# Performance work log

Hardware: AMD Instinct MI355X
Metric: run time of the kernel (lower is better)

## Reference

```python
import jax, jax.numpy as jnp
import numpy as np

N, E, H = 50000, 800000, 128
NUM_NC = 40
NUM_LAYERS = 3


def setup_inputs() -> dict:
    key = jax.random.key(0)
    ks = jax.random.split(key, 16)
    s = 1.0 / np.sqrt(H)
    inp = {
        "x": jax.random.normal(ks[0], (N, H), jnp.float32),
        "edge_index": jax.random.randint(ks[1], (2, E), 0, N, jnp.int64),
        "na_alphas": 0.001 * jax.random.normal(ks[2], (3, 4), jnp.float32),
        "sc_alphas": 0.001 * jax.random.normal(ks[3], (2, 2), jnp.float32),
        "la_alphas": 0.001 * jax.random.normal(ks[4], (1, 3), jnp.float32),
        "lin1_W": s * jax.random.normal(ks[5], (H, H), jnp.float32),
        "lin1_b": jnp.zeros((H,), jnp.float32),
        "gcn_W": s * jax.random.normal(ks[6], (3, H, H), jnp.float32),
        "gcn_b": jnp.zeros((3, H), jnp.float32),
        "sage_Ws": s * jax.random.normal(ks[7], (3, H, H), jnp.float32),
        "sage_Wn": s * jax.random.normal(ks[8], (3, H, H), jnp.float32),
        "gin_W": s * jax.random.normal(ks[9], (3, H, H), jnp.float32),
        "gin_b": jnp.zeros((3, H), jnp.float32),
        "gin_eps": jnp.zeros((3,), jnp.float32),
        "gat_W": s * jax.random.normal(ks[10], (3, H, H), jnp.float32),
        "gat_as": s * jax.random.normal(ks[11], (3, H), jnp.float32),
        "gat_ad": s * jax.random.normal(ks[12], (3, H), jnp.float32),
        "nc_W": s * jax.random.normal(ks[13], (NUM_NC, H), jnp.float32),
        "nc_b": jnp.zeros((NUM_NC,), jnp.float32),
    }
    return inp


def _gcn(x, src, dst, deg_inv_sqrt, W, b):
    h = x @ W.T + b                           # [N, H]
    norm = deg_inv_sqrt[src] * deg_inv_sqrt[dst]
    msg = h[src] * norm[:, None]              # [E, H] gather
    return jax.ops.segment_sum(msg, dst, num_segments=N)


def _sage(x, src, dst, deg, Ws, Wn):
    agg = jax.ops.segment_sum(x[src], dst, num_segments=N) / jnp.maximum(deg, 1.0)[:, None]
    return x @ Ws.T + agg @ Wn.T


def _gin(x, src, dst, W, b, eps):
    agg = jax.ops.segment_sum(x[src], dst, num_segments=N)
    return ((1.0 + eps) * x + agg) @ W.T + b


def _gat(x, src, dst, W, a_s, a_d):
    h = x @ W.T                               # [N, H]
    logits = jax.nn.leaky_relu((h @ a_s)[src] + (h @ a_d)[dst], 0.2)  # [E]
    m = jax.ops.segment_max(logits, dst, num_segments=N)
    e = jnp.exp(logits - m[dst])
    z = jax.ops.segment_sum(e, dst, num_segments=N)
    alpha = e / (z[dst] + 1e-16)
    return jax.ops.segment_sum(alpha[:, None] * h[src], dst, num_segments=N)


def _na_mixed(x, w, src, dst, deg, dis, l, gcn_W, gcn_b, sage_Ws, sage_Wn,
              gin_W, gin_b, gin_eps, gat_W, gat_as, gat_ad):
    # sum_i w_i * elu(op_i(x, edge_index))
    o0 = _gcn(x, src, dst, dis, gcn_W[l], gcn_b[l])
    o1 = _sage(x, src, dst, deg, sage_Ws[l], sage_Wn[l])
    o2 = _gin(x, src, dst, gin_W[l], gin_b[l], gin_eps[l])
    o3 = _gat(x, src, dst, gat_W[l], gat_as[l], gat_ad[l])
    return (w[0] * jax.nn.elu(o0) + w[1] * jax.nn.elu(o1)
            + w[2] * jax.nn.elu(o2) + w[3] * jax.nn.elu(o3))


def reference(x, edge_index, na_alphas, sc_alphas, la_alphas, lin1_W, lin1_b,
              gcn_W, gcn_b, sage_Ws, sage_Wn, gin_W, gin_b, gin_eps,
              gat_W, gat_as, gat_ad, nc_W, nc_b):
    src, dst = edge_index[0], edge_index[1]
    deg = jax.ops.segment_sum(jnp.ones((E,), x.dtype), dst, num_segments=N)
    dis = jnp.where(deg > 0, 1.0 / jnp.sqrt(jnp.maximum(deg, 1.0)), 0.0)

    na_w = jax.nn.softmax(na_alphas, axis=-1)   # [3, 4]
    sc_w = jax.nn.softmax(sc_alphas, axis=-1)   # [2, 2] (none, skip)
    la_w = jax.nn.softmax(la_alphas, axis=-1)   # [1, 3]

    h = x @ lin1_W.T + lin1_b                   # dropout: eval mode -> identity
    xs = []
    cur = h
    for l in range(NUM_LAYERS):
        cur = _na_mixed(cur, na_w[l], src, dst, deg, dis, l, gcn_W, gcn_b,
                        sage_Ws, sage_Wn, gin_W, gin_b, gin_eps,
                        gat_W, gat_as, gat_ad)
        xs.append(cur)
    x1, x2, x3 = xs

    # fix_last=True: x4 = (x3, sc0(x1), sc1(x2)); SC ops = {none->0, skip->id}
    t = jnp.stack([x3, sc_w[0, 1] * x1, sc_w[1, 1] * x2], axis=0)  # [3, N, H]

    # layer aggregator: sum_i w_i * relu(op_i(tuple)); ops = {max, mean, sum}
    x5 = (la_w[0, 0] * jax.nn.relu(jnp.max(t, axis=0))
          + la_w[0, 1] * jax.nn.relu(jnp.mean(t, axis=0))
          + la_w[0, 2] * jax.nn.relu(jnp.sum(t, axis=0)))

    return x5 @ nc_W.T + nc_b                   # [N, NUM_NC]
```

## Files before the change

kernel.cpp:

```cpp
#include <hip/hip_runtime.h>
#include <hip/hip_bf16.h>

typedef unsigned short u16;
typedef unsigned int u32;
typedef __attribute__((ext_vector_type(8))) short short8;
typedef __attribute__((ext_vector_type(4))) float f32x4;
typedef __attribute__((ext_vector_type(2))) float f32x2;

#define HD 128
#define ETILE 8192

__device__ inline float b2f(u16 u){ u32 v = ((u32)u) << 16; return __uint_as_float(v); }
__device__ inline u16 f2b(float f){
  u32 u = __float_as_uint(f);
  u32 r = (u + 0x7fffu + ((u >> 16) & 1u)) >> 16;
  return (u16)r;
}
__device__ inline u32 pack2(float a, float b){
  __hip_bfloat162 h = __float22bfloat162_rn(make_float2(a, b));
  union { __hip_bfloat162 h; u32 u; } c; c.h = h; return c.u;
}
__device__ inline float lo2f(u32 w){ return b2f((u16)(w & 0xffff)); }
__device__ inline float hi2f(u32 w){ return b2f((u16)(w >> 16)); }
__device__ inline float eluf(float x){ return x > 0.f ? x : __expf(x) - 1.f; }
__device__ inline float reluf(float x){ return x > 0.f ? x : 0.f; }
__device__ inline float sane(float x){
  if (!(x == x)) return 0.f;
  return fminf(fmaxf(x, -1e30f), 1e30f);
}
__device__ inline u32 fenc(float f){ u32 u = __float_as_uint(f); return (u & 0x80000000u) ? ~u : (u | 0x80000000u); }
__device__ inline float fdec(u32 u){ return __uint_as_float((u & 0x80000000u) ? (u & 0x7fffffffu) : ~u); }
__device__ __forceinline__ void async16(const u16* g, u16* l){
  __builtin_amdgcn_global_load_lds((const __attribute__((address_space(1))) void*)g,
                                   (__attribute__((address_space(3))) void*)l, 16, 0, 0);
}

__global__ void k_small(const float* __restrict__ na_a, const float* __restrict__ sc_a,
                        const float* __restrict__ la_a, const float* __restrict__ gatW,
                        const float* __restrict__ gat_as, const float* __restrict__ gat_ad,
                        const float* __restrict__ gin_eps, float* __restrict__ sm,
                        u32* __restrict__ maxs)
{
  int t = threadIdx.x;
  if (t < 3) maxs[t] = 0u;
  if (t == 0){
    for (int l = 0; l < 3; l++){
      float a[4]; float mx = -1e30f;
      for (int i = 0; i < 4; i++){ a[i] = na_a[l*4+i]; mx = fmaxf(mx, a[i]); }
      float ssum = 0.f;
      for (int i = 0; i < 4; i++){ a[i] = __expf(a[i]-mx); ssum += a[i]; }
      for (int i = 0; i < 4; i++) sm[l*4+i] = a[i]/ssum;
    }
    for (int r = 0; r < 2; r++){
      float a0 = sc_a[r*2], a1 = sc_a[r*2+1];
      float mx = fmaxf(a0,a1);
      float e0 = __expf(a0-mx), e1 = __expf(a1-mx);
      sm[12+r] = e1/(e0+e1);
    }
    {
      float a0=la_a[0], a1=la_a[1], a2=la_a[2];
      float mx = fmaxf(fmaxf(a0,a1),a2);
      float e0=__expf(a0-mx), e1=__expf(a1-mx), e2=__expf(a2-mx);
      float ssum = e0+e1+e2;
      sm[14]=e0/ssum; sm[15]=e1/ssum; sm[16]=e2/ssum;
    }
    for (int l=0;l<3;l++) sm[17+l] = 1.f + gin_eps[l];
  }
  if (t < 128){
    for (int l=0;l<3;l++){
      float a1=0.f, a2=0.f;
      for (int k=0;k<128;k++){
        float wv = gatW[l*16384 + k*128 + t];
        a1 = fmaf(wv, gat_as[l*128+k], a1);
        a2 = fmaf(wv, gat_ad[l*128+k], a2);
      }
      sm[32  + l*128 + t] = a1;
      sm[416 + l*128 + t] = a2;
    }
  }
}

__device__ __forceinline__ uint4 cvt8(const float* __restrict__ p){
  float4 v0 = *(const float4*)p;
  float4 v1 = *(const float4*)(p + 4);
  uint4 o;
  o.x = pack2(v0.x, v0.y);
  o.y = pack2(v0.z, v0.w);
  o.z = pack2(v1.x, v1.y);
  o.w = pack2(v1.z, v1.w);
  return o;
}
__global__ void k_wcvt(const float* __restrict__ lin1W, const float* __restrict__ gcnW,
                       const float* __restrict__ Ws, const float* __restrict__ Wn,
                       const float* __restrict__ ginW, const float* __restrict__ gatW,
                       u16* __restrict__ wsb)
{
  int i = blockIdx.x*256 + threadIdx.x;
  if (i >= 32768) return;
  int m = i >> 11;
  int j = i & 2047;
  int r = j >> 4, c = j & 15;
  const float* src;
  if (m == 0)       src = lin1W;
  else if (m < 4)   src = gcnW + (m-1)*16384;
  else if (m < 7)   src = Ws   + (m-4)*16384;
  else if (m < 10)  src = Wn   + (m-7)*16384;
  else if (m < 13)  src = ginW + (m-10)*16384;
  else              src = gatW + (m-13)*16384;
  int dj = r*16 + (c ^ (r & 15));
  *(uint4*)(wsb + ((size_t)m*2048 + dj)*8) = cvt8(src + r*HD + c*8);
}


__global__ void k_ehist(const int* __restrict__ ei, int E, int* __restrict__ eh){
  __shared__ int h[256];
  int t = threadIdx.x, b = blockIdx.x;
  h[t] = 0; __syncthreads();
  int base = b*ETILE;
  #pragma unroll
  for (int r = 0; r < ETILE/256; r++){
    int e = base + r*256 + t;
    if (e < E) atomicAdd(&h[ei[E + e] >> 8], 1);
  }
  __syncthreads();
  eh[b*256 + t] = h[t];
}
__global__ void k_escan(int* __restrict__ eh, int nblk, int* __restrict__ btot){
  __shared__ int s[256];
  int b = blockIdx.x, t = threadIdx.x;
  int carry = 0;
  int rounds = (nblk + 255)/256;
  for (int r = 0; r < rounds; r++){
    int i = r*256 + t;
    int v = (i < nblk) ? eh[i*256 + b] : 0;
    s[t] = v; __syncthreads();
    for (int off = 1; off < 256; off <<= 1){
      int a = (t >= off) ? s[t - off] : 0;
      __syncthreads();
      s[t] += a;
      __syncthreads();
    }
    if (i < nblk) eh[i*256 + b] = s[t] - v + carry;
    carry += s[255];
    __syncthreads();
  }
  if (t == 0) btot[b] = carry;
}
__global__ void k_bscan(const int* __restrict__ btot, int B, int E, int* __restrict__ bbase){
  __shared__ int s[256];
  int t = threadIdx.x;
  int v = (t < B) ? btot[t] : 0;
  s[t] = v; __syncthreads();
  for (int off = 1; off < 256; off <<= 1){
    int a = (t >= off) ? s[t - off] : 0;
    __syncthreads();
    s[t] += a;
    __syncthreads();
  }
  if (t < B) bbase[t] = s[t] - v;
  if (t == 0) bbase[B] = E;
}
__global__ void k_escat(const int* __restrict__ ei, int E, int B,
                        const int* __restrict__ eh, const int* __restrict__ bbase,
                        int2* __restrict__ ebuf){
  __shared__ int cur[256];
  int t = threadIdx.x, b = blockIdx.x;
  cur[t] = (t < B) ? bbase[t] + eh[b*256 + t] : 0;
  __syncthreads();
  int base = b*ETILE;
  #pragma unroll
  for (int r = 0; r < ETILE/256; r++){
    int e = base + r*256 + t;
    if (e < E){
      int sv = ei[e], dv = ei[E + e];
      int p = atomicAdd(&cur[dv >> 8], 1);
      ebuf[p] = make_int2(sv, dv);
    }
  }
}
__global__ void k_bcount(const int2* __restrict__ ebuf, const int* __restrict__ bbase,
                         int Nn, int* __restrict__ cnt){
  __shared__ int c[256];
  int t = threadIdx.x, b = blockIdx.x;
  c[t] = 0; __syncthreads();
  int beg = bbase[b], end2 = bbase[b+1];
  for (int i = beg + t; i < end2; i += 256)
    atomicAdd(&c[ebuf[i].y & 255], 1);
  __syncthreads();
  int node = b*256 + t;
  if (node < Nn) cnt[node] = c[t];
}
__global__ void k_bfill(const int2* __restrict__ ebuf, const int* __restrict__ bbase,
                        const int* __restrict__ rowptr, int Nn, int* __restrict__ csr){
  __shared__ int cu[256];
  int t = threadIdx.x, b = blockIdx.x;
  int node = b*256 + t;
  cu[t] = (node < Nn) ? rowptr[node] : 0;
  __syncthreads();
  int beg = bbase[b], end2 = bbase[b+1];
  for (int i = beg + t; i < end2; i += 256){
    int2 ed = ebuf[i];
    int p = atomicAdd(&cu[ed.y & 255], 1);
    csr[p] = ed.x;
  }
}

__global__ void k_scan1(const int* __restrict__ cnt, int Nn, int* __restrict__ bsum){
  __shared__ int red[256];
  int b = blockIdx.x, t = threadIdx.x;
  int base = b*1024 + t*4;
  int s = 0;
  #pragma unroll
  for (int k = 0; k < 4; k++){ int i = base + k; if (i < Nn) s += cnt[i]; }
  red[t] = s; __syncthreads();
  for (int off = 128; off; off >>= 1){
    if (t < off) red[t] += red[t + off];
    __syncthreads();
  }
  if (t == 0) bsum[b] = red[0];
}

__global__ void k_scan2(const int* __restrict__ bsum, int nb,
                        int* __restrict__ boffs, int* __restrict__ rowptr, int Nn){
  __shared__ int sc[1024];
  int t = threadIdx.x;
  int own = (t < nb) ? bsum[t] : 0;
  sc[t] = own;
  __syncthreads();
  for (int off = 1; off < 1024; off <<= 1){
    int add = (t >= off) ? sc[t - off] : 0;
    __syncthreads();
    sc[t] += add;
    __syncthreads();
  }
  if (t < nb) boffs[t] = sc[t] - own;
  if (t == 1023) rowptr[Nn] = sc[1023];
}

__global__ void k_scan3(const int* __restrict__ cnt, const int* __restrict__ boffs, int Nn,
                        int* __restrict__ rowptr, float4* __restrict__ nd){
  __shared__ int red[256];
  int b = blockIdx.x, t = threadIdx.x;
  int base = b*1024 + t*4;
  int c[4]; int s = 0;
  #pragma unroll
  for (int k = 0; k < 4; k++){ int i = base + k; c[k] = (i < Nn) ? cnt[i] : 0; s += c[k]; }
  red[t] = s; __syncthreads();
  for (int off = 1; off < 256; off <<= 1){
    int add = (t >= off) ? red[t - off] : 0;
    __syncthreads();
    red[t] += add;
    __syncthreads();
  }
  int run = red[t] - s + boffs[b];
  #pragma unroll
  for (int k = 0; k < 4; k++){
    int i = base + k;
    if (i < Nn){
      rowptr[i] = run;
      float f = (float)c[k];
      nd[i].z = c[k] > 0 ? 1.f/sqrtf(f) : 0.f;
      nd[i].w = 1.f/fmaxf(f, 1.f);
      run += c[k];
    }
  }
}

__global__ void k_histblk(const int* __restrict__ cnt, int Nn, int* __restrict__ bh){
  __shared__ int h[256];
  int t = threadIdx.x, b = blockIdx.x;
  h[t] = 0; __syncthreads();
  int base = b*1024;
  #pragma unroll
  for (int k = 0; k < 4; k++){
    int i = base + t + k*256;
    if (i < Nn){ int d = cnt[i]; if (d > 255) d = 255; atomicAdd(&h[d], 1); }
  }
  __syncthreads();
  bh[b*256 + t] = h[t];
}
__global__ void k_hsscan(int* __restrict__ bh, int nb){
  __shared__ int tot[256];
  __shared__ int sc[256];
  int t = threadIdx.x;
  int s = 0;
  for (int b = 0; b < nb; b++){
    int v = bh[b*256 + t];
    bh[b*256 + t] = s;
    s += v;
  }
  tot[t] = s;
  int rt = 255 - t;
  __syncthreads();
  sc[rt] = tot[t];
  __syncthreads();
  for (int off = 1; off < 256; off <<= 1){
    int a = (rt >= off) ? sc[rt - off] : 0;
    __syncthreads();
    sc[rt] += a;
    __syncthreads();
  }
  int binbase = sc[rt] - tot[t];
  for (int b = 0; b < nb; b++) bh[b*256 + t] += binbase;
}
__global__ void k_permscat(const int* __restrict__ cnt, int Nn,
                           const int* __restrict__ bh, int* __restrict__ perm){
  __shared__ int cur[256];
  int t = threadIdx.x, b = blockIdx.x;
  cur[t] = bh[b*256 + t];
  __syncthreads();
  int base = b*1024;
  #pragma unroll
  for (int k = 0; k < 4; k++){
    int i = base + t + k*256;
    if (i < Nn){
      int d = cnt[i]; if (d > 255) d = 255;
      int p = atomicAdd(&cur[d], 1);
      perm[p] = i;
    }
  }
}

__global__ __launch_bounds__(256)
void k_agg(const u16* __restrict__ X, const int* __restrict__ rowptr, const int* __restrict__ csr,
           const int* __restrict__ perm,
           const float4* __restrict__ nd, const float* __restrict__ sm,
           const u32* __restrict__ maxs, int layer, int Nn,
           u16* __restrict__ Qb, u16* __restrict__ Pm, u16* __restrict__ Gb, u16* __restrict__ Rb,
           float* __restrict__ b0)
{
  int tid = threadIdx.x;
  int lane = tid & 63;
  int g = lane >> 4, t = lane & 15;
  int idx = blockIdx.x*16 + (tid >> 6)*4 + g;
  if (idx >= Nn) return;
  int wv = perm[idx];
  int beg = rowptr[wv], end = rowptr[wv+1];
  float4 ndw = nd[wv];
  float dval = ndw.y;
  float bnd = fdec(maxs[layer]) + dval;
  float mloc = fmaxf(bnd, 0.2f*bnd);
  f32x2 p2[4], q2[4], r2[4];
  #pragma unroll
  for (int k = 0; k < 4; k++){ p2[k] = (f32x2){0.f,0.f}; q2[k] = (f32x2){0.f,0.f}; r2[k] = (f32x2){0.f,0.f}; }
  float z = 0.f, qd = 0.f;
  int e = beg;
  int nsv0=0, nsv1=0, nsv2=0, nsv3=0;
  if (e + 3 < end){ nsv0 = csr[e]; nsv1 = csr[e+1]; nsv2 = csr[e+2]; nsv3 = csr[e+3]; }
  while (e + 3 < end){
    int sv0 = nsv0, sv1 = nsv1, sv2 = nsv2, sv3 = nsv3;
    int en = e + 4;
    if (en + 3 < end){ nsv0 = csr[en]; nsv1 = csr[en+1]; nsv2 = csr[en+2]; nsv3 = csr[en+3]; }
    float4 n0 = nd[sv0], n1 = nd[sv1], n2 = nd[sv2], n3 = nd[sv3];
    uint4 xv0 = *(const uint4*)(X + (size_t)sv0*HD + (t ^ (sv0 & 15))*8);
    uint4 xv1 = *(const uint4*)(X + (size_t)sv1*HD + (t ^ (sv1 & 15))*8);
    uint4 xv2 = *(const uint4*)(X + (size_t)sv2*HD + (t ^ (sv2 & 15))*8);
    uint4 xv3 = *(const uint4*)(X + (size_t)sv3*HD + (t ^ (sv3 & 15))*8);
    float s0 = n0.x + dval, s1 = n1.x + dval, s2 = n2.x + dval, s3 = n3.x + dval;
    float lg0 = fmaxf(s0, 0.2f*s0), lg1 = fmaxf(s1, 0.2f*s1);
    float lg2 = fmaxf(s2, 0.2f*s2), lg3 = fmaxf(s3, 0.2f*s3);
    float ew0 = __expf(lg0 - mloc), ew1 = __expf(lg1 - mloc);
    float ew2 = __expf(lg2 - mloc), ew3 = __expf(lg3 - mloc);
    u32 a0[4] = {xv0.x, xv0.y, xv0.z, xv0.w};
    u32 a1[4] = {xv1.x, xv1.y, xv1.z, xv1.w};
    u32 a2[4] = {xv2.x, xv2.y, xv2.z, xv2.w};
    u32 a3[4] = {xv3.x, xv3.y, xv3.z, xv3.w};
    f32x2 d0 = {n0.z, n0.z}, d1 = {n1.z, n1.z}, d2 = {n2.z, n2.z}, d3 = {n3.z, n3.z};
    f32x2 e0 = {ew0, ew0}, e1v = {ew1, ew1}, e2v = {ew2, ew2}, e3v = {ew3, ew3};
    #pragma unroll
    for (int k = 0; k < 4; k++){
      f32x2 xf0 = {lo2f(a0[k]), hi2f(a0[k])};
      f32x2 xf1 = {lo2f(a1[k]), hi2f(a1[k])};
      f32x2 xf2 = {lo2f(a2[k]), hi2f(a2[k])};
      f32x2 xf3 = {lo2f(a3[k]), hi2f(a3[k])};
      p2[k] += (xf0 + xf1) + (xf2 + xf3);
      q2[k] = __builtin_elementwise_fma(xf0, d0, q2[k]);
      q2[k] = __builtin_elementwise_fma(xf1, d1, q2[k]);
      q2[k] = __builtin_elementwise_fma(xf2, d2, q2[k]);
      q2[k] = __builtin_elementwise_fma(xf3, d3, q2[k]);
      r2[k] = __builtin_elementwise_fma(xf0, e0, r2[k]);
      r2[k] = __builtin_elementwise_fma(xf1, e1v, r2[k]);
      r2[k] = __builtin_elementwise_fma(xf2, e2v, r2[k]);
      r2[k] = __builtin_elementwise_fma(xf3, e3v, r2[k]);
    }
    z += (ew0 + ew1) + (ew2 + ew3);
    qd += (n0.z + n1.z) + (n2.z + n3.z);
    e = en;
  }
  if (e + 1 < end){
    int sv0 = csr[e], sv1 = csr[e+1];
    float4 n0 = nd[sv0], n1 = nd[sv1];
    uint4 xv0 = *(const uint4*)(X + (size_t)sv0*HD + (t ^ (sv0 & 15))*8);
    uint4 xv1 = *(const uint4*)(X + (size_t)sv1*HD + (t ^ (sv1 & 15))*8);
    float s0 = n0.x + dval, s1 = n1.x + dval;
    float lg0 = fmaxf(s0, 0.2f*s0);
    float lg1 = fmaxf(s1, 0.2f*s1);
    float ew0 = __expf(lg0 - mloc), ew1 = __expf(lg1 - mloc);
    u32 a0[4] = {xv0.x, xv0.y, xv0.z, xv0.w};
    u32 a1[4] = {xv1.x, xv1.y, xv1.z, xv1.w};
    f32x2 d0 = {n0.z, n0.z}, d1 = {n1.z, n1.z};
    f32x2 e0 = {ew0, ew0},   e1v = {ew1, ew1};
    #pragma unroll
    for (int k = 0; k < 4; k++){
      f32x2 xf0 = {lo2f(a0[k]), hi2f(a0[k])};
      f32x2 xf1 = {lo2f(a1[k]), hi2f(a1[k])};
      p2[k] += xf0 + xf1;
      q2[k] = __builtin_elementwise_fma(xf0, d0, q2[k]);
      q2[k] = __builtin_elementwise_fma(xf1, d1, q2[k]);
      r2[k] = __builtin_elementwise_fma(xf0, e0, r2[k]);
      r2[k] = __builtin_elementwise_fma(xf1, e1v, r2[k]);
    }
    z += ew0 + ew1; qd += n0.z + n1.z;
    e += 2;
  }
  if (e < end){
    int sv = csr[e];
    float4 n0 = nd[sv];
    uint4 xv = *(const uint4*)(X + (size_t)sv*HD + (t ^ (sv & 15))*8);
    float s = n0.x + dval;
    float lg = fmaxf(s, 0.2f*s);
    float ew = __expf(lg - mloc);
    u32 a0[4] = {xv.x, xv.y, xv.z, xv.w};
    f32x2 d0 = {n0.z, n0.z}, e0 = {ew, ew};
    #pragma unroll
    for (int k = 0; k < 4; k++){
      f32x2 xf = {lo2f(a0[k]), hi2f(a0[k])};
      p2[k] += xf;
      q2[k] = __builtin_elementwise_fma(xf, d0, q2[k]);
      r2[k] = __builtin_elementwise_fma(xf, e0, r2[k]);
    }
    z += ew; qd += n0.z;
  }
  {
    float disv = ndw.z, dinvv = ndw.w;
    float zinv = 1.f/(z + 1e-16f);
    float e1 = sm[17 + layer];
    int tch = t ^ (wv & 15);
    size_t o = (size_t)wv*HD + tch*8;
    uint4 xo = *(const uint4*)(X + o);
    u32 ax[4] = {xo.x, xo.y, xo.z, xo.w};
    uint4 qo, po, go, ro;
    u32* qp = (u32*)&qo; u32* pp = (u32*)&po; u32* gp = (u32*)&go; u32* rp = (u32*)&ro;
    #pragma unroll
    for (int k = 0; k < 4; k++){
      float x0 = lo2f(ax[k]), x1 = hi2f(ax[k]);
      qp[k] = pack2(disv*q2[k].x, disv*q2[k].y);
      pp[k] = pack2(dinvv*p2[k].x, dinvv*p2[k].y);
      gp[k] = pack2(fmaf(e1, x0, p2[k].x), fmaf(e1, x1, p2[k].y));
      rp[k] = pack2(zinv*r2[k].x, zinv*r2[k].y);
    }
    *(uint4*)(Qb + o) = qo;
    *(uint4*)(Pm + o) = po;
    *(uint4*)(Gb + o) = go;
    *(uint4*)(Rb + o) = ro;
    if (t == 0) b0[wv] = disv*qd;
  }
}

__device__ __forceinline__ void stageB_async(u16* lds, const u16* __restrict__ w, int tid){
  int lane = tid & 63, wave = tid >> 6;
  #pragma unroll
  for (int i = 0; i < 8; i++){
    int cb = wave*64 + 256*i;
    async16(w + (size_t)(cb + lane)*8, lds + (size_t)cb*8);
  }
}
__device__ __forceinline__ void stageA64_f32(u16* lds, const float* __restrict__ src,
                                             int mbase, int Nn, int tid){
  #pragma unroll
  for (int i = 0; i < 4; i++){
    int chunk = tid + 256*i;
    int r = chunk >> 4;
    int c = chunk & 15;
    uint4 v = {0u,0u,0u,0u};
    int gr = mbase + r;
    if (gr < Nn) v = cvt8(src + (size_t)gr*HD + c*8);
    *(uint4*)(lds + (r*16 + (c ^ (r & 15)))*8) = v;
  }
}
__device__ __forceinline__ void mfma_tile64(const u16* Als, const u16* Bls,
                                            int m0, int lane, f32x4 acc[8]){
  int quad = lane >> 4, lr = lane & 15;
  #pragma unroll
  for (int ks = 0; ks < 4; ks++){
    int q = ks*4 + quad;
    short8 a, b[8];
    int row = m0 + lr;
    a = *(const short8*)(Als + (row*16 + (q ^ lr))*8);
    #pragma unroll
    for (int ct = 0; ct < 8; ct++){
      int brow = ct*16 + lr;
      b[ct] = *(const short8*)(Bls + (brow*16 + (q ^ lr))*8);
    }
    #pragma unroll
    for (int ct = 0; ct < 8; ct++)
      acc[ct] = __builtin_amdgcn_mfma_f32_16x16x32_bf16(a, b[ct], acc[ct], 0, 0, 0);
  }
}
__device__ __forceinline__ void mfma_regA(const short8 a[4], const u16* Bls,
                                          int lane, f32x4 acc[8]){
  int quad = lane >> 4, lr = lane & 15;
  #pragma unroll
  for (int ks = 0; ks < 4; ks++){
    int q = ks*4 + quad;
    short8 b[8];
    #pragma unroll
    for (int ct = 0; ct < 8; ct++)
      b[ct] = *(const short8*)(Bls + ((ct*16 + lr)*16 + (q ^ lr))*8);
    #pragma unroll
    for (int ct = 0; ct < 8; ct++)
      acc[ct] = __builtin_amdgcn_mfma_f32_16x16x32_bf16(a[ks], b[ct], acc[ct], 0, 0, 0);
  }
}

__global__ __launch_bounds__(256,3)
void k_gemm1(const float* __restrict__ A, const u16* __restrict__ Wb, const float* __restrict__ bias,
             const float* __restrict__ sm, float4* __restrict__ nd, u32* __restrict__ maxs,
             int Nn, u16* __restrict__ out)
{
  __shared__ __align__(16) u16 Als[64*128];
  __shared__ __align__(16) u16 Bls[128*128];
  __shared__ float mred[4];
  int tid = threadIdx.x;
  int lane = tid & 63, wave = tid >> 6;
  int m0 = wave*16, mbase = blockIdx.x*64;
  int quad = lane >> 4, lr = lane & 15;
  f32x4 acc[8];
  #pragma unroll
  for (int ct=0;ct<8;ct++) acc[ct] = (f32x4){0.f,0.f,0.f,0.f};
  stageB_async(Bls, Wb, tid);
  stageA64_f32(Als, A, mbase, Nn, tid);
  __syncthreads();
  mfma_tile64(Als, Bls, m0, lane, acc);
  #pragma unroll
  for (int ct=0;ct<8;ct++){
    float bc = bias[ct*16+lr];
    #pragma unroll
    for (int r=0;r<4;r++) acc[ct][r] = sane(acc[ct][r] + bc);
  }
  #pragma unroll
  for (int ct=0;ct<8;ct++){
    int c2 = ct*2 + (lr >> 3);
    #pragma unroll
    for (int r=0;r<4;r++){
      int grow = mbase + m0 + quad*4 + r;
      if (grow < Nn) out[(size_t)grow*HD + (c2 ^ (grow & 15))*8 + (lr & 7)] = f2b(acc[ct][r]);
    }
  }
  {
    const float* wsv = sm + 32;
    const float* wdv = sm + 416;
    float sp[4] = {0.f,0.f,0.f,0.f}, dp[4] = {0.f,0.f,0.f,0.f};
    #pragma unroll
    for (int ct=0;ct<8;ct++){
      float wsc = wsv[ct*16+lr], wdc = wdv[ct*16+lr];
      #pragma unroll
      for (int r=0;r<4;r++){
        sp[r] = fmaf(acc[ct][r], wsc, sp[r]);
        dp[r] = fmaf(acc[ct][r], wdc, dp[r]);
      }
    }
    #pragma unroll
    for (int off=1; off<16; off<<=1)
      #pragma unroll
      for (int r=0;r<4;r++){ sp[r] += __shfl_xor(sp[r], off); dp[r] += __shfl_xor(dp[r], off); }
    float ms = -3.4e38f;
    #pragma unroll
    for (int r=0;r<4;r++){
      int grow = mbase + m0 + quad*4 + r;
      if (grow < Nn){
        ms = fmaxf(ms, sp[r]);
        if (lr == 0) *(float2*)&nd[grow] = make_float2(sp[r], dp[r]);
      }
    }
    ms = fmaxf(ms, __shfl_xor(ms, 16));
    ms = fmaxf(ms, __shfl_xor(ms, 32));
    if (lane == 0) mred[wave] = ms;
    __syncthreads();
    if (tid == 0){
      float m = fmaxf(fmaxf(mred[0],mred[1]), fmaxf(mred[2],mred[3]));
      atomicMax(maxs + 0, fenc(m));
    }
  }
}

__global__ __launch_bounds__(256,2)
void k_layer3(const u16* __restrict__ X, const u16* __restrict__ Qb,
              const u16* __restrict__ Pm, const u16* __restrict__ Gb, const u16* __restrict__ Rb,
              float4* __restrict__ nd, const float* __restrict__ b0,
              const u16* __restrict__ wsb,
              const float* __restrict__ gcnB, const float* __restrict__ ginB,
              const float* __restrict__ sm, u32* __restrict__ maxs,
              int layer, int Nn, u16* __restrict__ out)
{
  __shared__ __align__(16) u16 Bls0[128*128];
  __shared__ __align__(16) u16 Bls1[128*128];
  __shared__ float mred[4];
  int tid = threadIdx.x;
  int lane = tid & 63, wave = tid >> 6;
  int m0 = wave*16, mbase = blockIdx.x*64;
  int quad = lane >> 4, lr = lane & 15;
  float w0 = sm[layer*4+0], w1 = sm[layer*4+1], w2 = sm[layer*4+2], w3 = sm[layer*4+3];
  const u16* gcnWb = wsb + (size_t)(1  + layer)*16384;
  const u16* WsWb  = wsb + (size_t)(4  + layer)*16384;
  const u16* WnWb  = wsb + (size_t)(7  + layer)*16384;
  const u16* ginWb = wsb + (size_t)(10 + layer)*16384;
  const u16* gatWb = wsb + (size_t)(13 + layer)*16384;

  int arow = mbase + m0 + lr; if (arow >= Nn) arow = Nn - 1;
  size_t abase = (size_t)arow * HD;
  int co[4];
  #pragma unroll
  for (int ks = 0; ks < 4; ks++) co[ks] = ((ks*4 + quad) ^ lr) * 8;

  f32x4 mix[8];
  f32x4 acc[8];
  float b0r[4];
  #pragma unroll
  for (int r=0;r<4;r++){
    int grow = mbase + m0 + quad*4 + r;
    b0r[r] = (grow < Nn) ? b0[grow] : 0.f;
  }

  short8 a0[4], a1[4];
  stageB_async(Bls0, gcnWb, tid);
  #pragma unroll
  for (int ks=0;ks<4;ks++) a0[ks] = *(const short8*)(Qb + abase + co[ks]);
  #pragma unroll
  for (int ks=0;ks<4;ks++) a1[ks] = *(const short8*)(X + abase + co[ks]);
  __syncthreads();

  stageB_async(Bls1, WsWb, tid);
  #pragma unroll
  for (int ct=0;ct<8;ct++) acc[ct] = (f32x4){0.f,0.f,0.f,0.f};
  mfma_regA(a0, Bls0, lane, acc);
  #pragma unroll
  for (int ks=0;ks<4;ks++) a0[ks] = *(const short8*)(Pm + abase + co[ks]);
  {
    float gb[8];
    #pragma unroll
    for (int ct=0;ct<8;ct++) gb[ct] = gcnB[layer*HD + ct*16+lr];
    #pragma unroll
    for (int ct=0;ct<8;ct++)
      #pragma unroll
      for (int r=0;r<4;r++)
        mix[ct][r] = w0 * eluf(acc[ct][r] + b0r[r]*gb[ct]);
  }
  __syncthreads();

  stageB_async(Bls0, WnWb, tid);
  #pragma unroll
  for (int ct=0;ct<8;ct++) acc[ct] = (f32x4){0.f,0.f,0.f,0.f};
  mfma_regA(a1, Bls1, lane, acc);
  #pragma unroll
  for (int ks=0;ks<4;ks++) a1[ks] = *(const short8*)(Gb + abase + co[ks]);
  __syncthreads();

  stageB_async(Bls1, ginWb, tid);
  mfma_regA(a0, Bls0, lane, acc);
  #pragma unroll
  for (int ks=0;ks<4;ks++) a0[ks] = *(const short8*)(Rb + abase + co[ks]);
  #pragma unroll
  for (int ct=0;ct<8;ct++)
    #pragma unroll
    for (int r=0;r<4;r++)
      mix[ct][r] += w1 * eluf(acc[ct][r]);
  __syncthreads();

  stageB_async(Bls0, gatWb, tid);
  #pragma unroll
  for (int ct=0;ct<8;ct++) acc[ct] = (f32x4){0.f,0.f,0.f,0.f};
  mfma_regA(a1, Bls1, lane, acc);
  {
    float gib[8];
    #pragma unroll
    for (int ct=0;ct<8;ct++) gib[ct] = ginB[layer*HD + ct*16+lr];
    #pragma unroll
    for (int ct=0;ct<8;ct++)
      #pragma unroll
      for (int r=0;r<4;r++)
        mix[ct][r] += w2 * eluf(acc[ct][r] + gib[ct]);
  }
  __syncthreads();

  #pragma unroll
  for (int ct=0;ct<8;ct++) acc[ct] = (f32x4){0.f,0.f,0.f,0.f};
  mfma_regA(a0, Bls0, lane, acc);
  #pragma unroll
  for (int ct=0;ct<8;ct++)
    #pragma unroll
    for (int r=0;r<4;r++)
      mix[ct][r] = sane(mix[ct][r] + w3 * eluf(acc[ct][r]));

  #pragma unroll
  for (int ct=0;ct<8;ct++){
    int c2 = ct*2 + (lr >> 3);
    #pragma unroll
    for (int r=0;r<4;r++){
      int grow = mbase + m0 + quad*4 + r;
      if (grow < Nn) out[(size_t)grow*HD + (c2 ^ (grow & 15))*8 + (lr & 7)] = f2b(mix[ct][r]);
    }
  }
  if (layer < 2){
    const float* wsv = sm + 32  + (layer+1)*128;
    const float* wdv = sm + 416 + (layer+1)*128;
    float sp[4] = {0.f,0.f,0.f,0.f}, dp[4] = {0.f,0.f,0.f,0.f};
    #pragma unroll
    for (int ct=0;ct<8;ct++){
      float wsc = wsv[ct*16+lr], wdc = wdv[ct*16+lr];
      #pragma unroll
      for (int r=0;r<4;r++){
        sp[r] = fmaf(mix[ct][r], wsc, sp[r]);
        dp[r] = fmaf(mix[ct][r], wdc, dp[r]);
      }
    }
    #pragma unroll
    for (int off=1; off<16; off<<=1)
      #pragma unroll
      for (int r=0;r<4;r++){ sp[r] += __shfl_xor(sp[r], off); dp[r] += __shfl_xor(dp[r], off); }
    float ms = -3.4e38f;
    #pragma unroll
    for (int r=0;r<4;r++){
      int grow = mbase + m0 + quad*4 + r;
      if (grow < Nn){
        ms = fmaxf(ms, sp[r]);
        if (lr == 0) *(float2*)&nd[grow] = make_float2(sp[r], dp[r]);
      }
    }
    ms = fmaxf(ms, __shfl_xor(ms, 16));
    ms = fmaxf(ms, __shfl_xor(ms, 32));
    if (lane == 0) mred[wave] = ms;
    __syncthreads();
    if (tid == 0){
      float m = fmaxf(fmaxf(mred[0],mred[1]), fmaxf(mred[2],mred[3]));
      atomicMax(maxs + layer + 1, fenc(m));
    }
  }
}

__global__ __launch_bounds__(256)
void k_nc(const u16* __restrict__ X1, const u16* __restrict__ X2, const u16* __restrict__ X3,
          const float* __restrict__ W, const float* __restrict__ bias,
          const float* __restrict__ sm, int Nn, float* __restrict__ out)
{
  __shared__ __align__(16) u16 xs[32*136];
  __shared__ __align__(16) float wn[40*132];
  __shared__ float bs[40];
  int t = threadIdx.x;
  int nb = blockIdx.x*32;
  float c1 = sm[12], c2 = sm[13], la0 = sm[14], la1 = sm[15], la2 = sm[16];
  #pragma unroll
  for (int i = 0; i < 2; i++){
    int chunk = t + 256*i;
    int r = chunk >> 4, c = chunk & 15;
    uint4 v = {0u,0u,0u,0u};
    int gr = nb + r;
    if (gr < Nn){
      size_t o = (size_t)gr*HD + ((c ^ (gr & 15))*8);
      uint4 u1 = *(const uint4*)(X1 + o);
      uint4 u2 = *(const uint4*)(X2 + o);
      uint4 u3 = *(const uint4*)(X3 + o);
      u32* u1p = (u32*)&u1; u32* u2p = (u32*)&u2; u32* u3p = (u32*)&u3; u32* vp = (u32*)&v;
      #pragma unroll
      for (int k = 0; k < 4; k++){
        float o0, o1;
        {
          float a1 = lo2f(u1p[k]), a2 = lo2f(u2p[k]), a3 = lo2f(u3p[k]);
          float t0 = a3, t1 = c1*a1, t2 = c2*a2;
          float smm = t0 + t1 + t2;
          float mx = fmaxf(fmaxf(t0,t1),t2);
          o0 = la0*reluf(mx) + la1*reluf(smm*(1.f/3.f)) + la2*reluf(smm);
        }
        {
          float a1 = hi2f(u1p[k]), a2 = hi2f(u2p[k]), a3 = hi2f(u3p[k]);
          float t0 = a3, t1 = c1*a1, t2 = c2*a2;
          float smm = t0 + t1 + t2;
          float mx = fmaxf(fmaxf(t0,t1),t2);
          o1 = la0*reluf(mx) + la1*reluf(smm*(1.f/3.f)) + la2*reluf(smm);
        }
        vp[k] = pack2(sane(o0), sane(o1));
      }
    }
    *(uint4*)(xs + r*136 + c*8) = v;
  }
  #pragma unroll
  for (int i = 0; i < 5; i++){
    int chunk = t + 256*i;
    int r = chunk >> 5, c = chunk & 31;
    *(float4*)(wn + r*132 + c*4) = *(const float4*)(W + r*HD + c*4);
  }
  if (t < 40) bs[t] = bias[t];
  __syncthreads();
  int nl = t >> 3, cg = t & 7;
  float acc[5];
  #pragma unroll
  for (int j = 0; j < 5; j++) acc[j] = bs[cg + 8*j];
  for (int k = 0; k < 128; k++){
    float xv = b2f(xs[nl*136 + k]);
    #pragma unroll
    for (int j = 0; j < 5; j++)
      acc[j] = fmaf(xv, wn[(cg + 8*j)*132 + k], acc[j]);
  }
  int gr = nb + nl;
  if (gr < Nn){
    #pragma unroll
    for (int j = 0; j < 5; j++)
      out[(size_t)gr*40 + cg + 8*j] = sane(acc[j]);
  }
}

extern "C" void kernel_launch(void* const* d_in, const int* in_sizes, int n_in,
                              void* d_out, int out_size, void* d_ws, size_t ws_size,
                              hipStream_t stream)
{
  (void)n_in; (void)out_size; (void)ws_size;
  const int N = in_sizes[0] / HD;
  const int E = in_sizes[1] / 2;
  const float* x      = (const float*)d_in[0];
  const int*   ei     = (const int*)d_in[1];
  const float* na_a   = (const float*)d_in[2];
  const float* sc_a   = (const float*)d_in[3];
  const float* la_a   = (const float*)d_in[4];
  const float* lin1W  = (const float*)d_in[5];
  const float* lin1b  = (const float*)d_in[6];
  const float* gcnW   = (const float*)d_in[7];
  const float* gcnB   = (const float*)d_in[8];
  const float* sageWs = (const float*)d_in[9];
  const float* sageWn = (const float*)d_in[10];
  const float* ginW   = (const float*)d_in[11];
  const float* ginB   = (const float*)d_in[12];
  const float* ginE   = (const float*)d_in[13];
  const float* gatW   = (const float*)d_in[14];
  const float* gatAs  = (const float*)d_in[15];
  const float* gatAd  = (const float*)d_in[16];
  const float* ncW    = (const float*)d_in[17];
  const float* ncB    = (const float*)d_in[18];

  char* base = (char*)d_ws;
  size_t off = 0;
  auto alloc = [&](size_t b) -> void* {
    void* p = base + off;
    off += (b + 255) & ~(size_t)255;
    return p;
  };
  const int NB  = (N + 1023) / 1024;
  const int B   = (N + 255) >> 8;
  const int nbe = (E + ETILE - 1) / ETILE;
  float*  smalls = (float*)alloc(4096);
  u32*    maxs   = (u32*)alloc(256);
  int*    cnt    = (int*)alloc((size_t)N*4);
  int*    rowptr = (int*)alloc(((size_t)N+1)*4);
  int*    bsum   = (int*)alloc(4096);
  int*    boffs  = (int*)alloc(4096);
  int*    bh     = (int*)alloc((size_t)NB*256*4);
  int*    perm   = (int*)alloc((size_t)N*4);
  int*    eh     = (int*)alloc((size_t)nbe*256*4);
  int*    btot   = (int*)alloc(1024);
  int*    bbase  = (int*)alloc(1040);
  float4* nd     = (float4*)alloc((size_t)N*16);
  float*  b0     = (float*)alloc((size_t)N*4);
  int*    csr    = (int*)alloc((size_t)E*4);
  u16*    wsb    = (u16*)alloc((size_t)16*16384*2);
  u16*    xh     = (u16*)alloc((size_t)N*HD*2);
  u16*    x1     = (u16*)alloc((size_t)N*HD*2);
  u16*    x2     = (u16*)alloc((size_t)N*HD*2);
  u16*    Qb     = (u16*)alloc((size_t)N*HD*2);
  u16*    Pm     = (u16*)alloc((size_t)N*HD*2);
  u16*    Gb     = (u16*)alloc((size_t)N*HD*2);
  u16*    Rb     = (u16*)alloc((size_t)N*HD*2);
  int2*   ebuf   = (int2*)Qb;

  k_small<<<1,128,0,stream>>>(na_a, sc_a, la_a, gatW, gatAs, gatAd, ginE, smalls, maxs);
  k_wcvt<<<128,256,0,stream>>>(lin1W, gcnW, sageWs, sageWn, ginW, gatW, wsb);
  k_ehist<<<nbe,256,0,stream>>>(ei, E, eh);
  k_escan<<<B,256,0,stream>>>(eh, nbe, btot);
  k_bscan<<<1,256,0,stream>>>(btot, B, E, bbase);
  k_escat<<<nbe,256,0,stream>>>(ei, E, B, eh, bbase, ebuf);
  k_bcount<<<B,256,0,stream>>>(ebuf, bbase, N, cnt);
  k_histblk<<<NB,256,0,stream>>>(cnt, N, bh);
  k_hsscan<<<1,256,0,stream>>>(bh, NB);
  k_permscat<<<NB,256,0,stream>>>(cnt, N, bh, perm);
  k_scan1<<<NB,256,0,stream>>>(cnt, N, bsum);
  k_scan2<<<1,1024,0,stream>>>(bsum, NB, boffs, rowptr, N);
  k_scan3<<<NB,256,0,stream>>>(cnt, boffs, N, rowptr, nd);
  k_bfill<<<B,256,0,stream>>>(ebuf, bbase, rowptr, N, csr);
  int gbl64 = (N + 63)/64;
  k_gemm1<<<gbl64,256,0,stream>>>(x, wsb, lin1b, smalls, nd, maxs, N, xh);
  const u16* xc = xh;
  u16* outs[3] = {x1, x2, xh};
  int abl = (N + 15)/16;
  for (int l = 0; l < 3; l++){
    k_agg<<<abl,256,0,stream>>>(xc, rowptr, csr, perm, nd, smalls, maxs, l, N, Qb, Pm, Gb, Rb, b0);
    k_layer3<<<gbl64,256,0,stream>>>(xc, Qb, Pm, Gb, Rb, nd, b0, wsb,
                                     gcnB, ginB, smalls, maxs, l, N, outs[l]);
    xc = outs[l];
  }
  int ncbl = (N + 31)/32;
  k_nc<<<ncbl,256,0,stream>>>(x1, x2, xh, ncW, ncB, smalls, N, (float*)d_out);
}
```

Before: 438.5 us.

## Derive SAGE mean and GIN input in layer kernel from one raw-sum buffer

The aggregation kernel now writes only three bf16 intermediates (GCN sum, raw neighbor sum, attention sum). It no longer writes separate mean and GIN buffers. The layer kernel rebuilds the SAGE mean by scaling the raw sum by 1/deg in registers, and the GIN input by combining it with the already-loaded self features. This cuts one N×H store per layer plus one load, and drops the extra X read in k_agg. In exchange, the layer kernel does some extra per-element conversion and uses more registers. The diff also makes k_gemm1 load A directly into registers instead of staging it through LDS, and shrinks ETILE for edge bucketing.

Measured after the change: 419.6 us. -4.3%, faster.

```diff
diff --git a/kernel.cpp b/kernel.cpp
--- a/kernel.cpp
+++ b/kernel.cpp
@@ -8,7 +8,7 @@
 typedef __attribute__((ext_vector_type(2))) float f32x2;
 
 #define HD 128
-#define ETILE 8192
+#define ETILE 2048
 
 __device__ inline float b2f(u16 u){ u32 v = ((u32)u) << 16; return __uint_as_float(v); }
 __device__ inline u16 f2b(float f){
@@ -33,6 +33,23 @@
 __device__ __forceinline__ void async16(const u16* g, u16* l){
   __builtin_amdgcn_global_load_lds((const __attribute__((address_space(1))) void*)g,
                                    (__attribute__((address_space(3))) void*)l, 16, 0, 0);
+}
+__device__ __forceinline__ short8 scale8(short8 v, float s){
+  union { short8 s8; u32 u[4]; } in, out;
+  in.s8 = v;
+  #pragma unroll
+  for (int i = 0; i < 4; i++)
+    out.u[i] = pack2(lo2f(in.u[i])*s, hi2f(in.u[i])*s);
+  return out.s8;
+}
+__device__ __forceinline__ short8 comb8(short8 x, short8 p, float e1){
+  union { short8 s8; u32 u[4]; } ux, up, out;
+  ux.s8 = x; up.s8 = p;
+  #pragma unroll
+  for (int i = 0; i < 4; i++)
+    out.u[i] = pack2(fmaf(e1, lo2f(ux.u[i]), lo2f(up.u[i])),
+                     fmaf(e1, hi2f(ux.u[i]), hi2f(up.u[i])));
+  return out.s8;
 }
 
 __global__ void k_small(const float* __restrict__ na_a, const float* __restrict__ sc_a,
@@ -326,7 +343,7 @@
            const int* __restrict__ perm,
            const float4* __restrict__ nd, const float* __restrict__ sm,
            const u32* __restrict__ maxs, int layer, int Nn,
-           u16* __restrict__ Qb, u16* __restrict__ Pm, u16* __restrict__ Gb, u16* __restrict__ Rb,
+           u16* __restrict__ Qb, u16* __restrict__ Pb, u16* __restrict__ Rb,
            float* __restrict__ b0)
 {
   int tid = threadIdx.x;
@@ -432,26 +449,20 @@
     z += ew; qd += n0.z;
   }
   {
-    float disv = ndw.z, dinvv = ndw.w;
+    float disv = ndw.z;
     float zinv = 1.f/(z + 1e-16f);
-    float e1 = sm[17 + layer];
     int tch = t ^ (wv & 15);
     size_t o = (size_t)wv*HD + tch*8;
-    uint4 xo = *(const uint4*)(X + o);
-    u32 ax[4] = {xo.x, xo.y, xo.z, xo.w};
-    uint4 qo, po, go, ro;
-    u32* qp = (u32*)&qo; u32* pp = (u32*)&po; u32* gp = (u32*)&go; u32* rp = (u32*)&ro;
+    uint4 qo, po, ro;
+    u32* qp = (u32*)&qo; u32* pp = (u32*)&po; u32* rp = (u32*)&ro;
     #pragma unroll
     for (int k = 0; k < 4; k++){
-      float x0 = lo2f(ax[k]), x1 = hi2f(ax[k]);
       qp[k] = pack2(disv*q2[k].x, disv*q2[k].y);
-      pp[k] = pack2(dinvv*p2[k].x, dinvv*p2[k].y);
-      gp[k] = pack2(fmaf(e1, x0, p2[k].x), fmaf(e1, x1, p2[k].y));
+      pp[k] = pack2(p2[k].x, p2[k].y);
       rp[k] = pack2(zinv*r2[k].x, zinv*r2[k].y);
     }
     *(uint4*)(Qb + o) = qo;
-    *(uint4*)(Pm + o) = po;
-    *(uint4*)(Gb + o) = go;
+    *(uint4*)(Pb + o) = po;
     *(uint4*)(Rb + o) = ro;
     if (t == 0) b0[wv] = disv*qd;
   }
@@ -463,38 +474,6 @@
   for (int i = 0; i < 8; i++){
     int cb = wave*64 + 256*i;
     async16(w + (size_t)(cb + lane)*8, lds + (size_t)cb*8);
-  }
-}
-__device__ __forceinline__ void stageA64_f32(u16* lds, const float* __restrict__ src,
-                                             int mbase, int Nn, int tid){
-  #pragma unroll
-  for (int i = 0; i < 4; i++){
-    int chunk = tid + 256*i;
-    int r = chunk >> 4;
-    int c = chunk & 15;
-    uint4 v = {0u,0u,0u,0u};
-    int gr = mbase + r;
-    if (gr < Nn) v = cvt8(src + (size_t)gr*HD + c*8);
-    *(uint4*)(lds + (r*16 + (c ^ (r & 15)))*8) = v;
-  }
-}
-__device__ __forceinline__ void mfma_tile64(const u16* Als, const u16* Bls,
-                                            int m0, int lane, f32x4 acc[8]){
-  int quad = lane >> 4, lr = lane & 15;
-  #pragma unroll
-  for (int ks = 0; ks < 4; ks++){
-    int q = ks*4 + quad;
-    short8 a, b[8];
-    int row = m0 + lr;
-    a = *(const short8*)(Als + (row*16 + (q ^ lr))*8);
-    #pragma unroll
-    for (int ct = 0; ct < 8; ct++){
-      int brow = ct*16 + lr;
-      b[ct] = *(const short8*)(Bls + (brow*16 + (q ^ lr))*8);
-    }
-    #pragma unroll
-    for (int ct = 0; ct < 8; ct++)
-      acc[ct] = __builtin_amdgcn_mfma_f32_16x16x32_bf16(a, b[ct], acc[ct], 0, 0, 0);
   }
 }
 __device__ __forceinline__ void mfma_regA(const short8 a[4], const u16* Bls,
@@ -518,20 +497,28 @@
              const float* __restrict__ sm, float4* __restrict__ nd, u32* __restrict__ maxs,
              int Nn, u16* __restrict__ out)
 {
-  __shared__ __align__(16) u16 Als[64*128];
   __shared__ __align__(16) u16 Bls[128*128];
   __shared__ float mred[4];
   int tid = threadIdx.x;
   int lane = tid & 63, wave = tid >> 6;
   int m0 = wave*16, mbase = blockIdx.x*64;
   int quad = lane >> 4, lr = lane & 15;
+  stageB_async(Bls, Wb, tid);
+  int arowi = mbase + m0 + lr;
+  int arow = (arowi < Nn) ? arowi : (Nn - 1);
+  short8 a[4];
+  #pragma unroll
+  for (int ks = 0; ks < 4; ks++){
+    int q = ks*4 + quad;
+    union { uint4 u; short8 s; } cv;
+    cv.u = cvt8(A + (size_t)arow*HD + q*8);
+    a[ks] = cv.s;
+  }
   f32x4 acc[8];
   #pragma unroll
   for (int ct=0;ct<8;ct++) acc[ct] = (f32x4){0.f,0.f,0.f,0.f};
-  stageB_async(Bls, Wb, tid);
-  stageA64_f32(Als, A, mbase, Nn, tid);
-  __syncthreads();
-  mfma_tile64(Als, Bls, m0, lane, acc);
+  __syncthreads();
+  mfma_regA(a, Bls, lane, acc);
   #pragma unroll
   for (int ct=0;ct<8;ct++){
     float bc = bias[ct*16+lr];
@@ -586,7 +573,7 @@
 
 __global__ __launch_bounds__(256,2)
 void k_layer3(const u16* __restrict__ X, const u16* __restrict__ Qb,
-              const u16* __restrict__ Pm, const u16* __restrict__ Gb, const u16* __restrict__ Rb,
+              const u16* __restrict__ Pb, const u16* __restrict__ Rb,
               float4* __restrict__ nd, const float* __restrict__ b0,
               const u16* __restrict__ wsb,
               const float* __restrict__ gcnB, const float* __restrict__ ginB,
@@ -601,17 +588,20 @@
   int m0 = wave*16, mbase = blockIdx.x*64;
   int quad = lane >> 4, lr = lane & 15;
   float w0 = sm[layer*4+0], w1 = sm[layer*4+1], w2 = sm[layer*4+2], w3 = sm[layer*4+3];
+  float e1 = sm[17 + layer];
   const u16* gcnWb = wsb + (size_t)(1  + layer)*16384;
   const u16* WsWb  = wsb + (size_t)(4  + layer)*16384;
   const u16* WnWb  = wsb + (size_t)(7  + layer)*16384;
   const u16* ginWb = wsb + (size_t)(10 + layer)*16384;
   const u16* gatWb = wsb + (size_t)(13 + layer)*16384;
 
-  int arow = mbase + m0 + lr; if (arow >= Nn) arow = Nn - 1;
+  int arowi = mbase + m0 + lr;
+  int arow = (arowi < Nn) ? arowi : (Nn - 1);
   size_t abase = (size_t)arow * HD;
   int co[4];
   #pragma unroll
   for (int ks = 0; ks < 4; ks++) co[ks] = ((ks*4 + quad) ^ lr) * 8;
+  float dvr = ((const float*)&nd[arow])[3];
 
   f32x4 mix[8];
   f32x4 acc[8];
@@ -622,20 +612,20 @@
     b0r[r] = (grow < Nn) ? b0[grow] : 0.f;
   }
 
-  short8 a0[4], a1[4];
+  short8 aQ[4], aX[4], aP[4], aR[4], aT[4];
   stageB_async(Bls0, gcnWb, tid);
   #pragma unroll
-  for (int ks=0;ks<4;ks++) a0[ks] = *(const short8*)(Qb + abase + co[ks]);
-  #pragma unroll
-  for (int ks=0;ks<4;ks++) a1[ks] = *(const short8*)(X + abase + co[ks]);
+  for (int ks=0;ks<4;ks++) aQ[ks] = *(const short8*)(Qb + abase + co[ks]);
+  #pragma unroll
+  for (int ks=0;ks<4;ks++) aX[ks] = *(const short8*)(X + abase + co[ks]);
   __syncthreads();
 
   stageB_async(Bls1, WsWb, tid);
   #pragma unroll
   for (int ct=0;ct<8;ct++) acc[ct] = (f32x4){0.f,0.f,0.f,0.f};
-  mfma_regA(a0, Bls0, lane, acc);
-  #pragma unroll
-  for (int ks=0;ks<4;ks++) a0[ks] = *(const short8*)(Pm + abase + co[ks]);
+  mfma_regA(aQ, Bls0, lane, acc);
+  #pragma unroll
+  for (int ks=0;ks<4;ks++) aP[ks] = *(const short8*)(Pb + abase + co[ks]);
   {
     float gb[8];
     #pragma unroll
@@ -651,15 +641,15 @@
   stageB_async(Bls0, WnWb, tid);
   #pragma unroll
   for (int ct=0;ct<8;ct++) acc[ct] = (f32x4){0.f,0.f,0.f,0.f};
-  mfma_regA(a1, Bls1, lane, acc);
-  #pragma unroll
-  for (int ks=0;ks<4;ks++) a1[ks] = *(const short8*)(Gb + abase + co[ks]);
+  mfma_regA(aX, Bls1, lane, acc);
+  #pragma unroll
+  for (int ks=0;ks<4;ks++) aR[ks] = *(const short8*)(Rb + abase + co[ks]);
   __syncthreads();
 
   stageB_async(Bls1, ginWb, tid);
-  mfma_regA(a0, Bls0, lane, acc);
-  #pragma unroll
-  for (int ks=0;ks<4;ks++) a0[ks] = *(const short8*)(Rb + abase + co[ks]);
+  #pragma unroll
+  for (int ks=0;ks<4;ks++) aT[ks] = scale8(aP[ks], dvr);
+  mfma_regA(aT, Bls0, lane, acc);
   #pragma unroll
   for (int ct=0;ct<8;ct++)
     #pragma unroll
@@ -669,8 +659,10 @@
 
   stageB_async(Bls0, gatWb, tid);
   #pragma unroll
+  for (int ks=0;ks<4;ks++) aT[ks] = comb8(aX[ks], aP[ks], e1);
+  #pragma unroll
   for (int ct=0;ct<8;ct++) acc[ct] = (f32x4){0.f,0.f,0.f,0.f};
-  mfma_regA(a1, Bls1, lane, acc);
+  mfma_regA(aT, Bls1, lane, acc);
   {
     float gib[8];
     #pragma unroll
@@ -685,7 +677,7 @@
 
   #pragma unroll
   for (int ct=0;ct<8;ct++) acc[ct] = (f32x4){0.f,0.f,0.f,0.f};
-  mfma_regA(a0, Bls0, lane, acc);
+  mfma_regA(aR, Bls0, lane, acc);
   #pragma unroll
   for (int ct=0;ct<8;ct++)
     #pragma unroll
@@ -865,8 +857,7 @@
   u16*    x1     = (u16*)alloc((size_t)N*HD*2);
   u16*    x2     = (u16*)alloc((size_t)N*HD*2);
   u16*    Qb     = (u16*)alloc((size_t)N*HD*2);
-  u16*    Pm     = (u16*)alloc((size_t)N*HD*2);
-  u16*    Gb     = (u16*)alloc((size_t)N*HD*2);
+  u16*    Pb     = (u16*)alloc((size_t)N*HD*2);
   u16*    Rb     = (u16*)alloc((size_t)N*HD*2);
   int2*   ebuf   = (int2*)Qb;
 
@@ -890,8 +881,8 @@
   u16* outs[3] = {x1, x2, xh};
   int abl = (N + 15)/16;
   for (int l = 0; l < 3; l++){
-    k_agg<<<abl,256,0,stream>>>(xc, rowptr, csr, perm, nd, smalls, maxs, l, N, Qb, Pm, Gb, Rb, b0);
-    k_layer3<<<gbl64,256,0,stream>>>(xc, Qb, Pm, Gb, Rb, nd, b0, wsb,
+    k_agg<<<abl,256,0,stream>>>(xc, rowptr, csr, perm, nd, smalls, maxs, l, N, Qb, Pb, Rb, b0);
+    k_layer3<<<gbl64,256,0,stream>>>(xc, Qb, Pb, Rb, nd, b0, wsb,
                                      gcnB, ginB, smalls, maxs, l, N, outs[l]);
     xc = outs[l];
   }
```
